# Optimization experiments

Hardware: AMD Instinct MI355X
Metric: run time of the kernel (lower is better)

Reference implementation:

```python
import jax, jax.numpy as jnp
import numpy as np

H = 128  # hidden_size

def setup_inputs() -> dict:
    key = jax.random.key(0)
    ks = jax.random.split(key, 12)
    B, SEQ = 256, 1000
    static = jax.random.normal(ks[0], (B, 2, SEQ), jnp.float32)
    dynamic = jax.random.uniform(ks[1], (B, 2, SEQ), jnp.float32)
    # Encoder = 1x1 Conv1d(in_ch -> H): weight (H, in_ch), bias (H,)
    def xavier(k, shape):
        fan_in, fan_out = shape[1], shape[0]
        lim = np.sqrt(6.0 / (fan_in + fan_out)).astype(np.float32)
        return jax.random.uniform(k, shape, jnp.float32, -lim, lim)
    enc_s_w = xavier(ks[2], (H, 2)); enc_s_b = jnp.zeros((H,), jnp.float32)
    enc_d_w = xavier(ks[3], (H, 2)); enc_d_b = jnp.zeros((H,), jnp.float32)
    v = xavier(ks[4], (1, H))[0]                 # attention vector (H,)
    W = xavier(ks[5], (H, 3 * H))                # attention matrix (H, 3H)
    dense_w = xavier(ks[6], (H, 128)); dense_b = jnp.zeros((H,), jnp.float32)
    lin_w = xavier(ks[7], (1, H)); lin_b = jnp.zeros((1,), jnp.float32)
    return {"static": static, "dynamic": dynamic,
            "enc_s_w": enc_s_w, "enc_s_b": enc_s_b,
            "enc_d_w": enc_d_w, "enc_d_b": enc_d_b,
            "v": v, "W": W,
            "dense_w": dense_w, "dense_b": dense_b,
            "lin_w": lin_w, "lin_b": lin_b}


def reference(static, dynamic, enc_s_w, enc_s_b, enc_d_w, enc_d_b,
              v, W, dense_w, dense_b, lin_w, lin_b):
    B = static.shape[0]
    # 1x1-conv encoders (computed once; identical across loop iterations)
    e = jnp.einsum('hc,bcs->bhs', enc_s_w, static) + enc_s_b[None, :, None]   # (B,H,S)
    dyn_ld = jnp.broadcast_to(dynamic[:, 1:2, :], dynamic.shape)              # load channel expanded
    d = jnp.einsum('hc,bcs->bhs', enc_d_w, dyn_ld) + enc_d_b[None, :, None]   # (B,H,S)
    hy = jnp.zeros((B, H), static.dtype)
    for _ in range(3):  # fixed 3-step refinement loop
        hidden = jnp.concatenate(
            [e, d, jnp.broadcast_to(hy[:, :, None], e.shape)], axis=1)        # (B,3H,S)
        u = jnp.tanh(jnp.einsum('hk,bks->bhs', W, hidden))                    # (B,H,S)
        logit = jnp.einsum('h,bhs->bs', v, u)                                 # (B,S)
        prob = jax.nn.softmax(logit, axis=-1)
        hy = jnp.einsum('bs,bhs->bh', prob, e)                                # context update
    out = jax.nn.relu(hy @ dense_w.T + dense_b) @ lin_w.T + lin_b             # (B,1)
    return out
```

## Files before the change

kernel.cpp:

```cpp
#include <hip/hip_runtime.h>
#include <math.h>

#define HH 128
#define SS 1000
#define NT 1024
#define NW (NT / 64)

#define C1 2.8853900817779268f
#define C2 1.4426950408889634f

__global__ void sc_precompute(const float* __restrict__ enc_s_w,
                              const float* __restrict__ enc_s_b,
                              const float* __restrict__ enc_d_w,
                              const float* __restrict__ enc_d_b,
                              const float* __restrict__ v,
                              const float* __restrict__ W,
                              float* __restrict__ ws) {
    int h = threadIdx.x;
    if (h >= HH) return;
    const float4* W1 = (const float4*)(W + h * (3 * HH));
    const float4* W2 = (const float4*)(W + h * (3 * HH) + HH);
    const float4* W3 = (const float4*)(W + h * (3 * HH) + 2 * HH);
    const float4* ES = (const float4*)enc_s_w;
    const float4* ED = (const float4*)enc_d_w;
    const float4* SB = (const float4*)enc_s_b;
    const float4* DB = (const float4*)enc_d_b;
    float a0 = 0.f, a1 = 0.f, ad = 0.f, cc = 0.f, w30 = 0.f, w31 = 0.f, w3b = 0.f;
    #pragma unroll 4
    for (int k4 = 0; k4 < HH / 4; ++k4) {
        float4 w1 = W1[k4], w2 = W2[k4], w3 = W3[k4];
        float4 e01 = ES[2 * k4], e23 = ES[2 * k4 + 1];
        float4 d01 = ED[2 * k4], d23 = ED[2 * k4 + 1];
        float4 sb = SB[k4], db = DB[k4];
        a0 = fmaf(w1.x, e01.x, a0); a0 = fmaf(w1.y, e01.z, a0);
        a0 = fmaf(w1.z, e23.x, a0); a0 = fmaf(w1.w, e23.z, a0);
        a1 = fmaf(w1.x, e01.y, a1); a1 = fmaf(w1.y, e01.w, a1);
        a1 = fmaf(w1.z, e23.y, a1); a1 = fmaf(w1.w, e23.w, a1);
        ad = fmaf(w2.x, d01.x + d01.y, ad); ad = fmaf(w2.y, d01.z + d01.w, ad);
        ad = fmaf(w2.z, d23.x + d23.y, ad); ad = fmaf(w2.w, d23.z + d23.w, ad);
        cc = fmaf(w1.x, sb.x, cc); cc = fmaf(w1.y, sb.y, cc);
        cc = fmaf(w1.z, sb.z, cc); cc = fmaf(w1.w, sb.w, cc);
        cc = fmaf(w2.x, db.x, cc); cc = fmaf(w2.y, db.y, cc);
        cc = fmaf(w2.z, db.z, cc); cc = fmaf(w2.w, db.w, cc);
        w30 = fmaf(w3.x, e01.x, w30); w30 = fmaf(w3.y, e01.z, w30);
        w30 = fmaf(w3.z, e23.x, w30); w30 = fmaf(w3.w, e23.z, w30);
        w31 = fmaf(w3.x, e01.y, w31); w31 = fmaf(w3.y, e01.w, w31);
        w31 = fmaf(w3.z, e23.y, w31); w31 = fmaf(w3.w, e23.w, w31);
        w3b = fmaf(w3.x, sb.x, w3b); w3b = fmaf(w3.y, sb.y, w3b);
        w3b = fmaf(w3.z, sb.z, w3b); w3b = fmaf(w3.w, sb.w, w3b);
    }
    ws[h]            = a0 * C1;
    ws[HH + h]       = a1 * C1;
    ws[2 * HH + h]   = ad * C1;
    ws[3 * HH + h]   = v[h];
    ws[4 * HH + h]   = cc * C1;
    ws[5 * HH + h]   = (cc + w3b) * C1;
    ws[6 * HH + h]   = w30 * C1;
    ws[7 * HH + h]   = w31 * C1;
    if (h == 0) {
        const float4* V4 = (const float4*)v;
        float s = 0.f;
        #pragma unroll 4
        for (int k = 0; k < HH / 4; ++k) { float4 t = V4[k]; s += t.x + t.y + t.z + t.w; }
        ws[8 * HH] = s * C2;
    }
}

template <int CTRL>
__device__ __forceinline__ float dpp_add(float x) {
    int s = __builtin_amdgcn_update_dpp(0, __builtin_bit_cast(int, x),
                                        CTRL, 0xF, 0xF, true);
    return x + __builtin_bit_cast(float, s);
}

__global__ __launch_bounds__(NT) void sc_main(
    const float* __restrict__ stat, const float* __restrict__ dyn,
    const float* __restrict__ ws,
    const float* __restrict__ enc_s_w, const float* __restrict__ enc_s_b,
    const float* __restrict__ dense_w, const float* __restrict__ dense_b,
    const float* __restrict__ lin_w, const float* __restrict__ lin_b,
    float* __restrict__ out) {
    const int b    = blockIdx.x;
    const int t    = threadIdx.x;
    const int wave = t >> 6;
    const int lane = t & 63;
    const int g    = t & 15;
    const int sg   = t >> 4;

    __shared__ __align__(16) float4 xs[NT];
    __shared__ float4 red4[2][NW];
    __shared__ __align__(16) float hy_sh[HH];

    {
        float x0 = 0.f, x1 = 0.f, yv = 0.f;
        if (t < SS) {
            const float* sb = stat + (size_t)b * 2 * SS;
            x0 = sb[t];
            x1 = sb[SS + t];
            yv = dyn[(size_t)b * 2 * SS + SS + t];
        }
        xs[t] = make_float4(x0, x1, yv, 0.f);
    }

    const int h0 = g * 8;
    float a0[8], a1[8], ad[8], vv[8], c0[8], cb[8], w0[8], w1[8];
    *(float4*)&a0[0] = *(const float4*)(ws + h0);
    *(float4*)&a0[4] = *(const float4*)(ws + h0 + 4);
    *(float4*)&a1[0] = *(const float4*)(ws + HH + h0);
    *(float4*)&a1[4] = *(const float4*)(ws + HH + h0 + 4);
    *(float4*)&ad[0] = *(const float4*)(ws + 2 * HH + h0);
    *(float4*)&ad[4] = *(const float4*)(ws + 2 * HH + h0 + 4);
    *(float4*)&vv[0] = *(const float4*)(ws + 3 * HH + h0);
    *(float4*)&vv[4] = *(const float4*)(ws + 3 * HH + h0 + 4);
    *(float4*)&c0[0] = *(const float4*)(ws + 4 * HH + h0);
    *(float4*)&c0[4] = *(const float4*)(ws + 4 * HH + h0 + 4);
    *(float4*)&cb[0] = *(const float4*)(ws + 5 * HH + h0);
    *(float4*)&cb[4] = *(const float4*)(ws + 5 * HH + h0 + 4);
    *(float4*)&w0[0] = *(const float4*)(ws + 6 * HH + h0);
    *(float4*)&w0[4] = *(const float4*)(ws + 6 * HH + h0 + 4);
    *(float4*)&w1[0] = *(const float4*)(ws + 7 * HH + h0);
    *(float4*)&w1[4] = *(const float4*)(ws + 7 * HH + h0 + 4);
    const float svc2 = ws[8 * HH];

    __syncthreads();

    float X0 = 0.f, X1 = 0.f;

    for (int iter = 0; iter < 3; ++iter) {
        float cg[8];
        #pragma unroll
        for (int i = 0; i < 8; ++i)
            cg[i] = (iter == 0) ? c0[i] : fmaf(w0[i], X0, fmaf(w1[i], X1, cb[i]));

        float S = 0.f, Sx0 = 0.f, Sx1 = 0.f;
        for (int pass = 0; pass < 16; ++pass) {
            const int s = pass * 64 + sg;
            float4 x = xs[s];
            float acc = 0.f;
            #pragma unroll
            for (int i = 0; i < 8; ++i) {
                float z = fmaf(a0[i], x.x, fmaf(a1[i], x.y, fmaf(ad[i], x.z, cg[i])));
                float e = __builtin_amdgcn_exp2f(z);
                acc = fmaf(vv[i], __builtin_amdgcn_rcpf(1.f + e), acc);
            }
            acc = dpp_add<0x118>(acc);
            acc = dpp_add<0x114>(acc);
            acc = dpp_add<0x112>(acc);
            acc = dpp_add<0x111>(acc);
            const bool own = (g == 15) && (s < SS);
            float arg = own ? fmaf(-C1, acc, svc2) : -128.f;
            float p = __builtin_amdgcn_exp2f(arg);
            S   += p;
            Sx0  = fmaf(p, x.x, Sx0);
            Sx1  = fmaf(p, x.y, Sx1);
        }

        S   += __shfl_xor(S, 16);   S   += __shfl_xor(S, 32);
        Sx0 += __shfl_xor(Sx0, 16); Sx0 += __shfl_xor(Sx0, 32);
        Sx1 += __shfl_xor(Sx1, 16); Sx1 += __shfl_xor(Sx1, 32);
        if (lane == 15) red4[iter & 1][wave] = make_float4(S, Sx0, Sx1, 0.f);
        __syncthreads();

        float4 w4 = red4[iter & 1][lane & 15];
        #pragma unroll
        for (int off = 1; off < 16; off <<= 1) {
            w4.x += __shfl_xor(w4.x, off);
            w4.y += __shfl_xor(w4.y, off);
            w4.z += __shfl_xor(w4.z, off);
        }
        float inv = __builtin_amdgcn_rcpf(w4.x);
        X0 = w4.y * inv;
        X1 = w4.z * inv;
    }

    if (t < HH)
        hy_sh[t] = fmaf(enc_s_w[2 * t], X0, fmaf(enc_s_w[2 * t + 1], X1, enc_s_b[t]));
    __syncthreads();

    float o = 0.f;
    if (t < HH) {
        const float4* dw4 = (const float4*)(dense_w + t * HH);
        const float4* hy4 = (const float4*)hy_sh;
        float r = dense_b[t];
        #pragma unroll 4
        for (int k = 0; k < HH / 4; ++k) {
            float4 d4 = dw4[k], h4 = hy4[k];
            r = fmaf(d4.x, h4.x, fmaf(d4.y, h4.y, fmaf(d4.z, h4.z, fmaf(d4.w, h4.w, r))));
        }
        o = lin_w[t] * fmaxf(r, 0.f);
    }
    #pragma unroll
    for (int off = 32; off > 0; off >>= 1) o += __shfl_xor(o, off);
    if (lane == 0) red4[0][wave].x = o;
    __syncthreads();
    if (t == 0) {
        float s = 0.f;
        for (int i = 0; i < NW; ++i) s += red4[0][i].x;
        out[b] = s + lin_b[0];
    }
}

extern "C" void kernel_launch(void* const* d_in, const int* in_sizes, int n_in,
                              void* d_out, int out_size, void* d_ws, size_t ws_size,
                              hipStream_t stream) {
    const float* stat    = (const float*)d_in[0];
    const float* dyn     = (const float*)d_in[1];
    const float* enc_s_w = (const float*)d_in[2];
    const float* enc_s_b = (const float*)d_in[3];
    const float* enc_d_w = (const float*)d_in[4];
    const float* enc_d_b = (const float*)d_in[5];
    const float* v       = (const float*)d_in[6];
    const float* W       = (const float*)d_in[7];
    const float* dense_w = (const float*)d_in[8];
    const float* dense_b = (const float*)d_in[9];
    const float* lin_w   = (const float*)d_in[10];
    const float* lin_b   = (const float*)d_in[11];
    float* out = (float*)d_out;
    float* ws  = (float*)d_ws;

    const int B = in_sizes[0] / (2 * SS);

    hipLaunchKernelGGL(sc_precompute, dim3(1), dim3(HH), 0, stream,
                       enc_s_w, enc_s_b, enc_d_w, enc_d_b, v, W, ws);
    hipLaunchKernelGGL(sc_main, dim3(B), dim3(NT), 0, stream,
                       stat, dyn, ws, enc_s_w, enc_s_b, dense_w, dense_b,
                       lin_w, lin_b, out);
}
```

Baseline: 48.52 us.

## Fuse weight precompute into main kernel and use packed-FP32 with 4 h per lane

Removes the single-block precompute launch. Each block now recomputes the folded weight vectors cooperatively, 8 threads per hidden unit with a DPP reduction, and stages them in LDS. The main loop changes to 32 lanes per sequence position with 4 hidden units each, computed with 2-wide packed FMA vectors, and the cross-lane reduction grows to cover 32 lanes. This removes a launch and its serialization but makes every block redundantly read W.

Result: slower. 50.30 us (+3.7%).

```diff
diff --git a/kernel.cpp b/kernel.cpp
--- a/kernel.cpp
+++ b/kernel.cpp
@@ -9,62 +9,7 @@
 #define C1 2.8853900817779268f
 #define C2 1.4426950408889634f
 
-__global__ void sc_precompute(const float* __restrict__ enc_s_w,
-                              const float* __restrict__ enc_s_b,
-                              const float* __restrict__ enc_d_w,
-                              const float* __restrict__ enc_d_b,
-                              const float* __restrict__ v,
-                              const float* __restrict__ W,
-                              float* __restrict__ ws) {
-    int h = threadIdx.x;
-    if (h >= HH) return;
-    const float4* W1 = (const float4*)(W + h * (3 * HH));
-    const float4* W2 = (const float4*)(W + h * (3 * HH) + HH);
-    const float4* W3 = (const float4*)(W + h * (3 * HH) + 2 * HH);
-    const float4* ES = (const float4*)enc_s_w;
-    const float4* ED = (const float4*)enc_d_w;
-    const float4* SB = (const float4*)enc_s_b;
-    const float4* DB = (const float4*)enc_d_b;
-    float a0 = 0.f, a1 = 0.f, ad = 0.f, cc = 0.f, w30 = 0.f, w31 = 0.f, w3b = 0.f;
-    #pragma unroll 4
-    for (int k4 = 0; k4 < HH / 4; ++k4) {
-        float4 w1 = W1[k4], w2 = W2[k4], w3 = W3[k4];
-        float4 e01 = ES[2 * k4], e23 = ES[2 * k4 + 1];
-        float4 d01 = ED[2 * k4], d23 = ED[2 * k4 + 1];
-        float4 sb = SB[k4], db = DB[k4];
-        a0 = fmaf(w1.x, e01.x, a0); a0 = fmaf(w1.y, e01.z, a0);
-        a0 = fmaf(w1.z, e23.x, a0); a0 = fmaf(w1.w, e23.z, a0);
-        a1 = fmaf(w1.x, e01.y, a1); a1 = fmaf(w1.y, e01.w, a1);
-        a1 = fmaf(w1.z, e23.y, a1); a1 = fmaf(w1.w, e23.w, a1);
-        ad = fmaf(w2.x, d01.x + d01.y, ad); ad = fmaf(w2.y, d01.z + d01.w, ad);
-        ad = fmaf(w2.z, d23.x + d23.y, ad); ad = fmaf(w2.w, d23.z + d23.w, ad);
-        cc = fmaf(w1.x, sb.x, cc); cc = fmaf(w1.y, sb.y, cc);
-        cc = fmaf(w1.z, sb.z, cc); cc = fmaf(w1.w, sb.w, cc);
-        cc = fmaf(w2.x, db.x, cc); cc = fmaf(w2.y, db.y, cc);
-        cc = fmaf(w2.z, db.z, cc); cc = fmaf(w2.w, db.w, cc);
-        w30 = fmaf(w3.x, e01.x, w30); w30 = fmaf(w3.y, e01.z, w30);
-        w30 = fmaf(w3.z, e23.x, w30); w30 = fmaf(w3.w, e23.z, w30);
-        w31 = fmaf(w3.x, e01.y, w31); w31 = fmaf(w3.y, e01.w, w31);
-        w31 = fmaf(w3.z, e23.y, w31); w31 = fmaf(w3.w, e23.w, w31);
-        w3b = fmaf(w3.x, sb.x, w3b); w3b = fmaf(w3.y, sb.y, w3b);
-        w3b = fmaf(w3.z, sb.z, w3b); w3b = fmaf(w3.w, sb.w, w3b);
-    }
-    ws[h]            = a0 * C1;
-    ws[HH + h]       = a1 * C1;
-    ws[2 * HH + h]   = ad * C1;
-    ws[3 * HH + h]   = v[h];
-    ws[4 * HH + h]   = cc * C1;
-    ws[5 * HH + h]   = (cc + w3b) * C1;
-    ws[6 * HH + h]   = w30 * C1;
-    ws[7 * HH + h]   = w31 * C1;
-    if (h == 0) {
-        const float4* V4 = (const float4*)v;
-        float s = 0.f;
-        #pragma unroll 4
-        for (int k = 0; k < HH / 4; ++k) { float4 t = V4[k]; s += t.x + t.y + t.z + t.w; }
-        ws[8 * HH] = s * C2;
-    }
-}
+typedef float v2f __attribute__((ext_vector_type(2)));
 
 template <int CTRL>
 __device__ __forceinline__ float dpp_add(float x) {
@@ -73,10 +18,11 @@
     return x + __builtin_bit_cast(float, s);
 }
 
-__global__ __launch_bounds__(NT) void sc_main(
+__global__ __launch_bounds__(NT) void sc_fused(
     const float* __restrict__ stat, const float* __restrict__ dyn,
-    const float* __restrict__ ws,
     const float* __restrict__ enc_s_w, const float* __restrict__ enc_s_b,
+    const float* __restrict__ enc_d_w, const float* __restrict__ enc_d_b,
+    const float* __restrict__ v, const float* __restrict__ W,
     const float* __restrict__ dense_w, const float* __restrict__ dense_b,
     const float* __restrict__ lin_w, const float* __restrict__ lin_b,
     float* __restrict__ out) {
@@ -84,12 +30,14 @@
     const int t    = threadIdx.x;
     const int wave = t >> 6;
     const int lane = t & 63;
-    const int g    = t & 15;
-    const int sg   = t >> 4;
+    const int g    = t & 31;
+    const int sg   = t >> 5;
 
     __shared__ __align__(16) float4 xs[NT];
+    __shared__ __align__(16) float kc[8][HH];
     __shared__ float4 red4[2][NW];
-    __shared__ __align__(16) float hy_sh[HH];
+    __shared__ float hy_sh[HH];
+    __shared__ float svc2_sh;
 
     {
         float x0 = 0.f, x1 = 0.f, yv = 0.f;
@@ -102,65 +50,142 @@
         xs[t] = make_float4(x0, x1, yv, 0.f);
     }
 
-    const int h0 = g * 8;
-    float a0[8], a1[8], ad[8], vv[8], c0[8], cb[8], w0[8], w1[8];
-    *(float4*)&a0[0] = *(const float4*)(ws + h0);
-    *(float4*)&a0[4] = *(const float4*)(ws + h0 + 4);
-    *(float4*)&a1[0] = *(const float4*)(ws + HH + h0);
-    *(float4*)&a1[4] = *(const float4*)(ws + HH + h0 + 4);
-    *(float4*)&ad[0] = *(const float4*)(ws + 2 * HH + h0);
-    *(float4*)&ad[4] = *(const float4*)(ws + 2 * HH + h0 + 4);
-    *(float4*)&vv[0] = *(const float4*)(ws + 3 * HH + h0);
-    *(float4*)&vv[4] = *(const float4*)(ws + 3 * HH + h0 + 4);
-    *(float4*)&c0[0] = *(const float4*)(ws + 4 * HH + h0);
-    *(float4*)&c0[4] = *(const float4*)(ws + 4 * HH + h0 + 4);
-    *(float4*)&cb[0] = *(const float4*)(ws + 5 * HH + h0);
-    *(float4*)&cb[4] = *(const float4*)(ws + 5 * HH + h0 + 4);
-    *(float4*)&w0[0] = *(const float4*)(ws + 6 * HH + h0);
-    *(float4*)&w0[4] = *(const float4*)(ws + 6 * HH + h0 + 4);
-    *(float4*)&w1[0] = *(const float4*)(ws + 7 * HH + h0);
-    *(float4*)&w1[4] = *(const float4*)(ws + 7 * HH + h0 + 4);
-    const float svc2 = ws[8 * HH];
-
+    {
+        const int fh = t >> 3;
+        const int fq = t & 7;
+        const float4* W1 = (const float4*)(W + fh * (3 * HH));
+        const float4* W2 = (const float4*)(W + fh * (3 * HH) + HH);
+        const float4* W3 = (const float4*)(W + fh * (3 * HH) + 2 * HH);
+        const float4* ES = (const float4*)enc_s_w;
+        const float4* ED = (const float4*)enc_d_w;
+        const float4* SB = (const float4*)enc_s_b;
+        const float4* DB = (const float4*)enc_d_b;
+        float a0 = 0.f, a1 = 0.f, ad = 0.f, cc = 0.f, w30 = 0.f, w31 = 0.f, w3b = 0.f;
+        #pragma unroll
+        for (int j = 0; j < 4; ++j) {
+            const int k4 = fq * 4 + j;
+            float4 w1 = W1[k4], w2 = W2[k4], w3 = W3[k4];
+            float4 e01 = ES[2 * k4], e23 = ES[2 * k4 + 1];
+            float4 d01 = ED[2 * k4], d23 = ED[2 * k4 + 1];
+            float4 sb = SB[k4], db = DB[k4];
+            a0 = fmaf(w1.x, e01.x, a0); a0 = fmaf(w1.y, e01.z, a0);
+            a0 = fmaf(w1.z, e23.x, a0); a0 = fmaf(w1.w, e23.z, a0);
+            a1 = fmaf(w1.x, e01.y, a1); a1 = fmaf(w1.y, e01.w, a1);
+            a1 = fmaf(w1.z, e23.y, a1); a1 = fmaf(w1.w, e23.w, a1);
+            ad = fmaf(w2.x, d01.x + d01.y, ad); ad = fmaf(w2.y, d01.z + d01.w, ad);
+            ad = fmaf(w2.z, d23.x + d23.y, ad); ad = fmaf(w2.w, d23.z + d23.w, ad);
+            cc = fmaf(w1.x, sb.x, cc); cc = fmaf(w1.y, sb.y, cc);
+            cc = fmaf(w1.z, sb.z, cc); cc = fmaf(w1.w, sb.w, cc);
+            cc = fmaf(w2.x, db.x, cc); cc = fmaf(w2.y, db.y, cc);
+            cc = fmaf(w2.z, db.z, cc); cc = fmaf(w2.w, db.w, cc);
+            w30 = fmaf(w3.x, e01.x, w30); w30 = fmaf(w3.y, e01.z, w30);
+            w30 = fmaf(w3.z, e23.x, w30); w30 = fmaf(w3.w, e23.z, w30);
+            w31 = fmaf(w3.x, e01.y, w31); w31 = fmaf(w3.y, e01.w, w31);
+            w31 = fmaf(w3.z, e23.y, w31); w31 = fmaf(w3.w, e23.w, w31);
+            w3b = fmaf(w3.x, sb.x, w3b); w3b = fmaf(w3.y, sb.y, w3b);
+            w3b = fmaf(w3.z, sb.z, w3b); w3b = fmaf(w3.w, sb.w, w3b);
+        }
+        a0  = dpp_add<0x111>(a0);  a0  = dpp_add<0x112>(a0);  a0  = dpp_add<0x114>(a0);
+        a1  = dpp_add<0x111>(a1);  a1  = dpp_add<0x112>(a1);  a1  = dpp_add<0x114>(a1);
+        ad  = dpp_add<0x111>(ad);  ad  = dpp_add<0x112>(ad);  ad  = dpp_add<0x114>(ad);
+        cc  = dpp_add<0x111>(cc);  cc  = dpp_add<0x112>(cc);  cc  = dpp_add<0x114>(cc);
+        w30 = dpp_add<0x111>(w30); w30 = dpp_add<0x112>(w30); w30 = dpp_add<0x114>(w30);
+        w31 = dpp_add<0x111>(w31); w31 = dpp_add<0x112>(w31); w31 = dpp_add<0x114>(w31);
+        w3b = dpp_add<0x111>(w3b); w3b = dpp_add<0x112>(w3b); w3b = dpp_add<0x114>(w3b);
+        if (fq == 7) {
+            kc[0][fh] = a0 * C1;
+            kc[1][fh] = a1 * C1;
+            kc[2][fh] = ad * C1;
+            kc[4][fh] = cc * C1;
+            kc[5][fh] = (cc + w3b) * C1;
+            kc[6][fh] = w30 * C1;
+            kc[7][fh] = w31 * C1;
+        }
+        if (t < HH) kc[3][t] = v[t];
+        if (t < 32) {
+            float4 x = ((const float4*)v)[t];
+            float s = (x.x + x.y) + (x.z + x.w);
+            #pragma unroll
+            for (int off = 1; off < 32; off <<= 1) s += __shfl_xor(s, off);
+            if (t == 0) svc2_sh = s * C2;
+        }
+    }
     __syncthreads();
 
+    const int h4 = g * 4;
+    float4 u;
+    u = *(const float4*)&kc[0][h4]; const v2f a0_0 = {u.x, u.y}, a0_1 = {u.z, u.w};
+    u = *(const float4*)&kc[1][h4]; const v2f a1_0 = {u.x, u.y}, a1_1 = {u.z, u.w};
+    u = *(const float4*)&kc[2][h4]; const v2f ad_0 = {u.x, u.y}, ad_1 = {u.z, u.w};
+    u = *(const float4*)&kc[3][h4]; const v2f vv_0 = {u.x, u.y}, vv_1 = {u.z, u.w};
+    const float svc2 = svc2_sh;
+    const v2f one2 = {1.f, 1.f};
+    const bool owner = (g == 31);
+
     float X0 = 0.f, X1 = 0.f;
 
     for (int iter = 0; iter < 3; ++iter) {
-        float cg[8];
-        #pragma unroll
-        for (int i = 0; i < 8; ++i)
-            cg[i] = (iter == 0) ? c0[i] : fmaf(w0[i], X0, fmaf(w1[i], X1, cb[i]));
+        v2f cg_0, cg_1;
+        if (iter == 0) {
+            u = *(const float4*)&kc[4][h4];
+            cg_0 = (v2f){u.x, u.y};
+            cg_1 = (v2f){u.z, u.w};
+        } else {
+            float4 ub = *(const float4*)&kc[5][h4];
+            float4 u0 = *(const float4*)&kc[6][h4];
+            float4 u1 = *(const float4*)&kc[7][h4];
+            v2f X0v = {X0, X0}, X1v = {X1, X1};
+            cg_0 = __builtin_elementwise_fma(
+                (v2f){u0.x, u0.y}, X0v,
+                __builtin_elementwise_fma((v2f){u1.x, u1.y}, X1v, (v2f){ub.x, ub.y}));
+            cg_1 = __builtin_elementwise_fma(
+                (v2f){u0.z, u0.w}, X0v,
+                __builtin_elementwise_fma((v2f){u1.z, u1.w}, X1v, (v2f){ub.z, ub.w}));
+        }
 
         float S = 0.f, Sx0 = 0.f, Sx1 = 0.f;
-        for (int pass = 0; pass < 16; ++pass) {
-            const int s = pass * 64 + sg;
+        #pragma unroll 2
+        for (int pass = 0; pass < 32; ++pass) {
+            const int s = pass * 32 + sg;
             float4 x = xs[s];
-            float acc = 0.f;
-            #pragma unroll
-            for (int i = 0; i < 8; ++i) {
-                float z = fmaf(a0[i], x.x, fmaf(a1[i], x.y, fmaf(ad[i], x.z, cg[i])));
-                float e = __builtin_amdgcn_exp2f(z);
-                acc = fmaf(vv[i], __builtin_amdgcn_rcpf(1.f + e), acc);
-            }
+            v2f vx0 = {x.x, x.x}, vx1 = {x.y, x.y}, vyv = {x.z, x.z};
+            v2f z0 = __builtin_elementwise_fma(
+                a0_0, vx0, __builtin_elementwise_fma(
+                    a1_0, vx1, __builtin_elementwise_fma(ad_0, vyv, cg_0)));
+            v2f z1 = __builtin_elementwise_fma(
+                a0_1, vx0, __builtin_elementwise_fma(
+                    a1_1, vx1, __builtin_elementwise_fma(ad_1, vyv, cg_1)));
+            v2f e0, e1;
+            e0.x = __builtin_amdgcn_exp2f(z0.x);
+            e0.y = __builtin_amdgcn_exp2f(z0.y);
+            e1.x = __builtin_amdgcn_exp2f(z1.x);
+            e1.y = __builtin_amdgcn_exp2f(z1.y);
+            v2f d0 = e0 + one2, d1 = e1 + one2;
+            v2f r0, r1;
+            r0.x = __builtin_amdgcn_rcpf(d0.x);
+            r0.y = __builtin_amdgcn_rcpf(d0.y);
+            r1.x = __builtin_amdgcn_rcpf(d1.x);
+            r1.y = __builtin_amdgcn_rcpf(d1.y);
+            v2f acc2 = __builtin_elementwise_fma(vv_0, r0, (v2f){0.f, 0.f});
+            acc2 = __builtin_elementwise_fma(vv_1, r1, acc2);
+            float acc = acc2.x + acc2.y;
+            acc = dpp_add<0x111>(acc);
+            acc = dpp_add<0x112>(acc);
+            acc = dpp_add<0x114>(acc);
             acc = dpp_add<0x118>(acc);
-            acc = dpp_add<0x114>(acc);
-            acc = dpp_add<0x112>(acc);
-            acc = dpp_add<0x111>(acc);
-            const bool own = (g == 15) && (s < SS);
-            float arg = own ? fmaf(-C1, acc, svc2) : -128.f;
+            acc = dpp_add<0x142>(acc);
+            const bool own = owner && (s < SS);
+            float arg = own ? fmaf(-C1, acc, svc2) : -200.f;
             float p = __builtin_amdgcn_exp2f(arg);
             S   += p;
             Sx0  = fmaf(p, x.x, Sx0);
             Sx1  = fmaf(p, x.y, Sx1);
         }
-
-        S   += __shfl_xor(S, 16);   S   += __shfl_xor(S, 32);
-        Sx0 += __shfl_xor(Sx0, 16); Sx0 += __shfl_xor(Sx0, 32);
-        Sx1 += __shfl_xor(Sx1, 16); Sx1 += __shfl_xor(Sx1, 32);
-        if (lane == 15) red4[iter & 1][wave] = make_float4(S, Sx0, Sx1, 0.f);
+        S   += __shfl_xor(S, 32);
+        Sx0 += __shfl_xor(Sx0, 32);
+        Sx1 += __shfl_xor(Sx1, 32);
+        if (lane == 31) red4[iter & 1][wave] = make_float4(S, Sx0, Sx1, 0.f);
         __syncthreads();
-
         float4 w4 = red4[iter & 1][lane & 15];
         #pragma unroll
         for (int off = 1; off < 16; off <<= 1) {
@@ -184,8 +209,8 @@
         float r = dense_b[t];
         #pragma unroll 4
         for (int k = 0; k < HH / 4; ++k) {
-            float4 d4 = dw4[k], h4 = hy4[k];
-            r = fmaf(d4.x, h4.x, fmaf(d4.y, h4.y, fmaf(d4.z, h4.z, fmaf(d4.w, h4.w, r))));
+            float4 d4 = dw4[k], h4v = hy4[k];
+            r = fmaf(d4.x, h4v.x, fmaf(d4.y, h4v.y, fmaf(d4.z, h4v.z, fmaf(d4.w, h4v.w, r))));
         }
         o = lin_w[t] * fmaxf(r, 0.f);
     }
@@ -216,13 +241,10 @@
     const float* lin_w   = (const float*)d_in[10];
     const float* lin_b   = (const float*)d_in[11];
     float* out = (float*)d_out;
-    float* ws  = (float*)d_ws;
 
     const int B = in_sizes[0] / (2 * SS);
 
-    hipLaunchKernelGGL(sc_precompute, dim3(1), dim3(HH), 0, stream,
-                       enc_s_w, enc_s_b, enc_d_w, enc_d_b, v, W, ws);
-    hipLaunchKernelGGL(sc_main, dim3(B), dim3(NT), 0, stream,
-                       stat, dyn, ws, enc_s_w, enc_s_b, dense_w, dense_b,
-                       lin_w, lin_b, out);
+    hipLaunchKernelGGL(sc_fused, dim3(B), dim3(NT), 0, stream,
+                       stat, dyn, enc_s_w, enc_s_b, enc_d_w, enc_d_b, v, W,
+                       dense_w, dense_b, lin_w, lin_b, out);
 }
```
